# Performance work log

Measured on AMD Instinct MI355X. Metric: run time of the kernel, lower is better.

## Reference

```python
import jax, jax.numpy as jnp
import numpy as np

B, N, IN_DIM, OUT_DIM, H = 8, 1024, 256, 256, 8
D = OUT_DIM // H  # support_dim = 32


def setup_inputs() -> dict:
    key = jax.random.key(0)
    k_a, k_x, k_w, k_f1, k_f2 = jax.random.split(key, 5)
    A = (jax.random.uniform(k_a, (B, N, N)) < 0.05).astype(jnp.float32)
    eye = jnp.eye(N, dtype=jnp.float32)
    A = jnp.maximum(A, eye[None, :, :])
    X = jax.random.normal(k_x, (B, N, IN_DIM), dtype=jnp.float32)
    std_w = 1.0 / np.sqrt(OUT_DIM)
    std_f = 1.0 / np.sqrt(D)
    weight = jax.random.uniform(k_w, (IN_DIM, OUT_DIM), minval=-std_w, maxval=std_w)
    fc1 = jax.random.uniform(k_f1, (H, D), minval=-std_f, maxval=std_f)
    fc2 = jax.random.uniform(k_f2, (H, D), minval=-std_f, maxval=std_f)
    return {"A": A, "X": X, "weight": weight, "fc1": fc1, "fc2": fc2}


def reference(A, X, weight, fc1, fc2):
    # inputs: [B, N, H, D]
    inputs = jnp.einsum('bni,io->bno', X, weight).reshape(B, N, H, D)
    # additive attention scores (rank-1 broadcast)
    self_s = jnp.einsum('bnhd,hd->bhn', inputs, fc1)   # [B,H,N] (query/self term)
    neigh_s = jnp.einsum('bnhd,hd->bhn', inputs, fc2)  # [B,H,N] (key/neighbor term)
    scores = jax.nn.leaky_relu(self_s[:, :, :, None] + neigh_s[:, :, None, :])  # [B,H,N,N]
    mask = (-1e9 * (1.0 - A))[:, None, :, :]  # [B,1,N,N]
    alphas = jax.nn.softmax(scores + mask, axis=-1)  # [B,H,N,N]
    out = jnp.einsum('bhnm,bmhd->bnhd', alphas, inputs).reshape(B, N, OUT_DIM)
    return jax.nn.relu(out)
```

## Files before the change

kernel.cpp:

```cpp
#include <hip/hip_runtime.h>

typedef unsigned short u16;
typedef __attribute__((ext_vector_type(8))) short short8;
typedef __attribute__((ext_vector_type(4))) float floatx4;

#define NB 8
#define NN 1024
#define KDIM 256
#define ODIM 256
#define NH 8
#define BR 32
#define LDA 264
#define GWPB 4
#define GCAP 192

__device__ __forceinline__ u16 bf_rne(float x) {
    union { float f; unsigned u; } c{x};
    unsigned r = c.u + 0x7fff + ((c.u >> 16) & 1);
    return (u16)(r >> 16);
}
__device__ __forceinline__ float bf_f(u16 b) {
    union { unsigned u; float f; } c{(unsigned)b << 16};
    return c.f;
}
#define SPLIT1(val, A_, B_) { u16 hh_ = bf_rne(val); u16 ll_ = bf_rne((val) - bf_f(hh_)); A_ = hh_; B_ = ll_; }

__global__ __launch_bounds__(256) void wprep(const float* __restrict__ W,
                                             u16* __restrict__ WhiT,
                                             u16* __restrict__ WloT) {
    __shared__ float tile[64][65];
    int bt = blockIdx.x;
    int kt = bt >> 2, ot = bt & 3;
    int tid = threadIdx.x;
    int r = tid >> 6, c = tid & 63;
#pragma unroll
    for (int rr = r; rr < 64; rr += 4)
        tile[rr][c] = W[(kt * 64 + rr) * ODIM + ot * 64 + c];
    __syncthreads();
#pragma unroll
    for (int oo = r; oo < 64; oo += 4) {
        float w = tile[c][oo];
        u16 h, l;
        SPLIT1(w, h, l)
        WhiT[(ot * 64 + oo) * KDIM + kt * 64 + c] = h;
        WloT[(ot * 64 + oo) * KDIM + kt * 64 + c] = l;
    }
}

__global__ __launch_bounds__(256) void gemm_scores(
        const float* __restrict__ X, const u16* __restrict__ WhiT,
        const u16* __restrict__ WloT, const float* __restrict__ fc1,
        const float* __restrict__ fc2, u16* __restrict__ inp,
        float* __restrict__ self_t, float* __restrict__ neigh_t) {
    __shared__ u16 ah_lds[BR * LDA];
    __shared__ u16 al_lds[BR * LDA];

    int tid = threadIdx.x;
    int w = tid >> 6, lane = tid & 63;
    int m = lane & 15, q = lane >> 4;
    int bid = blockIdx.x;
    int row0 = (bid >> 1) * BR;
    int cbase = (bid & 1) * 128;

    const float4* Xr = (const float4*)(X + (size_t)row0 * KDIM);
#pragma unroll
    for (int p = 0; p < 8; ++p) {
        int f = p * 256 + tid;
        int r = f >> 6, c4 = (f & 63) * 4;
        float4 v = Xr[f];
        ushort4 hi, lo;
        SPLIT1(v.x, hi.x, lo.x)
        SPLIT1(v.y, hi.y, lo.y)
        SPLIT1(v.z, hi.z, lo.z)
        SPLIT1(v.w, hi.w, lo.w)
        *(ushort4*)&ah_lds[r * LDA + c4] = hi;
        *(ushort4*)&al_lds[r * LDA + c4] = lo;
    }
    __syncthreads();

    floatx4 acc[2][2] = {{{0,0,0,0},{0,0,0,0}},{{0,0,0,0},{0,0,0,0}}};
#pragma unroll
    for (int k0 = 0; k0 < KDIM; k0 += 32) {
        short8 Ah0 = *(const short8*)&ah_lds[m * LDA + k0 + q * 8];
        short8 Al0 = *(const short8*)&al_lds[m * LDA + k0 + q * 8];
        short8 Ah1 = *(const short8*)&ah_lds[(16 + m) * LDA + k0 + q * 8];
        short8 Al1 = *(const short8*)&al_lds[(16 + m) * LDA + k0 + q * 8];
#pragma unroll
        for (int t = 0; t < 2; ++t) {
            int o = cbase + w * 32 + t * 16 + m;
            short8 Bh = *(const short8*)(WhiT + (size_t)o * KDIM + k0 + q * 8);
            short8 Bl = *(const short8*)(WloT + (size_t)o * KDIM + k0 + q * 8);
            acc[0][t] = __builtin_amdgcn_mfma_f32_16x16x32_bf16(Ah0, Bh, acc[0][t], 0, 0, 0);
            acc[0][t] = __builtin_amdgcn_mfma_f32_16x16x32_bf16(Ah0, Bl, acc[0][t], 0, 0, 0);
            acc[0][t] = __builtin_amdgcn_mfma_f32_16x16x32_bf16(Al0, Bh, acc[0][t], 0, 0, 0);
            acc[1][t] = __builtin_amdgcn_mfma_f32_16x16x32_bf16(Ah1, Bh, acc[1][t], 0, 0, 0);
            acc[1][t] = __builtin_amdgcn_mfma_f32_16x16x32_bf16(Ah1, Bl, acc[1][t], 0, 0, 0);
            acc[1][t] = __builtin_amdgcn_mfma_f32_16x16x32_bf16(Al1, Bh, acc[1][t], 0, 0, 0);
        }
    }

#pragma unroll
    for (int rt = 0; rt < 2; ++rt)
#pragma unroll
        for (int t = 0; t < 2; ++t) {
            int col = cbase + w * 32 + t * 16 + m;
#pragma unroll
            for (int r = 0; r < 4; ++r)
                inp[(size_t)(row0 + rt * 16 + q * 4 + r) * ODIM + col] =
                    bf_rne(acc[rt][t][r]);
        }

    int hd = (bid & 1) * 4 + w;
    float f1[2], f2[2];
#pragma unroll
    for (int t = 0; t < 2; ++t) {
        int cl = hd * 32 + t * 16 + m;
        f1[t] = fc1[cl];
        f2[t] = fc2[cl];
    }
#pragma unroll
    for (int rt = 0; rt < 2; ++rt)
#pragma unroll
        for (int r = 0; r < 4; ++r) {
            float a = acc[rt][0][r] * f1[0] + acc[rt][1][r] * f1[1];
            float bb = acc[rt][0][r] * f2[0] + acc[rt][1][r] * f2[1];
#pragma unroll
            for (int ofs = 8; ofs >= 1; ofs >>= 1) {
                a += __shfl_xor(a, ofs);
                bb += __shfl_xor(bb, ofs);
            }
            if (m == 0) {
                int n = row0 + rt * 16 + q * 4 + r;
                self_t [(size_t)n * NH + hd] = a;
                neigh_t[(size_t)n * NH + hd] = bb;
            }
        }
}

__global__ __launch_bounds__(256) void gat_agg(
        const float* __restrict__ A, const u16* __restrict__ inp,
        const float* __restrict__ self_t, const float* __restrict__ neigh_t,
        float* __restrict__ out) {
    __shared__ u16 lst[GWPB][GCAP];

    int tid = threadIdx.x;
    int wv = tid >> 6, lane = tid & 63;
    int bx = blockIdx.x;
    int b = bx & 7;
    int n = ((bx >> 3) << 2) | wv;
    int bn = (b << 10) | n;

    const float4* Ar = (const float4*)(A + (size_t)bn * NN);
    float4 ac0 = Ar[lane];
    float4 ac1 = Ar[64 + lane];
    float4 ac2 = Ar[128 + lane];
    float4 ac3 = Ar[192 + lane];

    unsigned long long lt = (1ull << lane) - 1;
    u16* L = lst[wv];
    int total = 0;

#define COMPACT(V, EIDX) {                                                   \
        unsigned long long mk_ = __ballot((V) != 0.f);                       \
        if ((V) != 0.f) {                                                    \
            int p_ = total + __popcll(mk_ & lt);                             \
            if (p_ < GCAP) L[p_] = (u16)(EIDX);                              \
        }                                                                    \
        total += __popcll(mk_); }

    {
        int e0 = lane * 4;
        COMPACT(ac0.x, e0)       COMPACT(ac0.y, e0 + 1)
        COMPACT(ac0.z, e0 + 2)   COMPACT(ac0.w, e0 + 3)
        COMPACT(ac1.x, 256 + e0) COMPACT(ac1.y, 256 + e0 + 1)
        COMPACT(ac1.z, 256 + e0 + 2) COMPACT(ac1.w, 256 + e0 + 3)
        COMPACT(ac2.x, 512 + e0) COMPACT(ac2.y, 512 + e0 + 1)
        COMPACT(ac2.z, 512 + e0 + 2) COMPACT(ac2.w, 512 + e0 + 3)
        COMPACT(ac3.x, 768 + e0) COMPACT(ac3.y, 768 + e0 + 1)
        COMPACT(ac3.z, 768 + e0 + 2) COMPACT(ac3.w, 768 + e0 + 3)
    }
#undef COMPACT
    if (total > GCAP) total = GCAP;

    int hh = lane >> 3;
    float selfv = self_t[(size_t)bn * NH + hh];
    const float* nst = neigh_t + (size_t)(b << 10) * NH + hh;
    const ushort4* ib = (const ushort4*)(inp + ((size_t)(b << 10)) * ODIM) + lane;
    float sum = 0.f;
    floatx4 acc = {0.f, 0.f, 0.f, 0.f};
#pragma unroll 4
    for (int i = 0; i < total; ++i) {
        int idx = L[i];
        float s = selfv + nst[(size_t)idx * NH];
        s = s > 0.f ? s : 0.01f * s;
        float e = __expf(s);
        sum += e;
        ushort4 v = ib[(size_t)idx * 64];
        acc[0] = fmaf(e, bf_f(v.x), acc[0]);
        acc[1] = fmaf(e, bf_f(v.y), acc[1]);
        acc[2] = fmaf(e, bf_f(v.z), acc[2]);
        acc[3] = fmaf(e, bf_f(v.w), acc[3]);
    }

    float inv = 1.f / sum;
    float4 o;
    o.x = acc[0] * inv; o.y = acc[1] * inv;
    o.z = acc[2] * inv; o.w = acc[3] * inv;
    o.x = o.x > 0.f ? o.x : 0.f;
    o.y = o.y > 0.f ? o.y : 0.f;
    o.z = o.z > 0.f ? o.z : 0.f;
    o.w = o.w > 0.f ? o.w : 0.f;
    *(float4*)(out + (size_t)bn * ODIM + lane * 4) = o;
}

extern "C" void kernel_launch(void* const* d_in, const int* in_sizes, int n_in,
                              void* d_out, int out_size, void* d_ws, size_t ws_size,
                              hipStream_t stream) {
    const float* A   = (const float*)d_in[0];
    const float* X   = (const float*)d_in[1];
    const float* W   = (const float*)d_in[2];
    const float* fc1 = (const float*)d_in[3];
    const float* fc2 = (const float*)d_in[4];
    float* out = (float*)d_out;

    char* ws = (char*)d_ws;
    const size_t MB = 1024u * 1024u;
    u16*   inp     = (u16*)ws;
    u16*   WhiT    = (u16*)(ws + 4 * MB);
    u16*   WloT    = (u16*)(ws + 4 * MB + 128 * 1024);
    float* self_t  = (float*)(ws + 4 * MB + 256 * 1024);
    float* neigh_t = (float*)(ws + 4 * MB + 512 * 1024);

    wprep<<<16, 256, 0, stream>>>(W, WhiT, WloT);
    gemm_scores<<<(NB * NN / BR) * 2, 256, 0, stream>>>(
        X, WhiT, WloT, fc1, fc2, inp, self_t, neigh_t);
    gat_agg<<<NB * NN / GWPB, 256, 0, stream>>>(A, inp, self_t, neigh_t, out);
}
```

Baseline: 123.2 us.

## Fuse weight prep, GEMM and aggregation into one cooperative persistent kernel

Merges the three kernels into a single cooperative launch of 512 blocks separated by grid-wide syncs, so there is only one kernel launch. The aggregation phase now has each wave handle four rows in sequence, prefetching the next adjacency row while the current one is compacted and aggregated. This removes inter-kernel launch gaps but adds grid barrier cost, leaves most blocks idle during the weight-prep phase, and reduces parallelism in the aggregation phase.

```diff
diff --git a/kernel.cpp b/kernel.cpp
--- a/kernel.cpp
+++ b/kernel.cpp
@@ -1,4 +1,7 @@
 #include <hip/hip_runtime.h>
+#include <hip/hip_cooperative_groups.h>
+
+namespace cg = cooperative_groups;
 
 typedef unsigned short u16;
 typedef __attribute__((ext_vector_type(8))) short short8;
@@ -11,7 +14,6 @@
 #define NH 8
 #define BR 32
 #define LDA 264
-#define GWPB 4
 #define GCAP 192
 
 __device__ __forceinline__ u16 bf_rne(float x) {
@@ -25,192 +27,200 @@
 }
 #define SPLIT1(val, A_, B_) { u16 hh_ = bf_rne(val); u16 ll_ = bf_rne((val) - bf_f(hh_)); A_ = hh_; B_ = ll_; }
 
-__global__ __launch_bounds__(256) void wprep(const float* __restrict__ W,
-                                             u16* __restrict__ WhiT,
-                                             u16* __restrict__ WloT) {
-    __shared__ float tile[64][65];
-    int bt = blockIdx.x;
-    int kt = bt >> 2, ot = bt & 3;
+__global__ __launch_bounds__(256, 2) void gat_fused(
+        const float* __restrict__ A, const float* __restrict__ X,
+        const float* __restrict__ W, const float* __restrict__ fc1,
+        const float* __restrict__ fc2, u16* __restrict__ inp,
+        u16* __restrict__ WhiT, u16* __restrict__ WloT,
+        float* __restrict__ self_t, float* __restrict__ neigh_t,
+        float* __restrict__ out) {
+    __shared__ __align__(16) char smem[2 * BR * LDA * 2];
+
     int tid = threadIdx.x;
-    int r = tid >> 6, c = tid & 63;
-#pragma unroll
-    for (int rr = r; rr < 64; rr += 4)
-        tile[rr][c] = W[(kt * 64 + rr) * ODIM + ot * 64 + c];
-    __syncthreads();
-#pragma unroll
-    for (int oo = r; oo < 64; oo += 4) {
-        float w = tile[c][oo];
-        u16 h, l;
-        SPLIT1(w, h, l)
-        WhiT[(ot * 64 + oo) * KDIM + kt * 64 + c] = h;
-        WloT[(ot * 64 + oo) * KDIM + kt * 64 + c] = l;
+    int bid = blockIdx.x;
+    int w = tid >> 6, lane = tid & 63;
+
+    if (bid < 16) {
+        float (*tile)[65] = (float(*)[65])smem;
+        int kt = bid >> 2, ot = bid & 3;
+        int r = tid >> 6, c = tid & 63;
+#pragma unroll
+        for (int rr = r; rr < 64; rr += 4)
+            tile[rr][c] = W[(kt * 64 + rr) * ODIM + ot * 64 + c];
+        __syncthreads();
+#pragma unroll
+        for (int oo = r; oo < 64; oo += 4) {
+            float wv_ = tile[c][oo];
+            u16 h, l;
+            SPLIT1(wv_, h, l)
+            WhiT[(ot * 64 + oo) * KDIM + kt * 64 + c] = h;
+            WloT[(ot * 64 + oo) * KDIM + kt * 64 + c] = l;
+        }
+        __threadfence();
     }
-}
-
-__global__ __launch_bounds__(256) void gemm_scores(
-        const float* __restrict__ X, const u16* __restrict__ WhiT,
-        const u16* __restrict__ WloT, const float* __restrict__ fc1,
-        const float* __restrict__ fc2, u16* __restrict__ inp,
-        float* __restrict__ self_t, float* __restrict__ neigh_t) {
-    __shared__ u16 ah_lds[BR * LDA];
-    __shared__ u16 al_lds[BR * LDA];
-
-    int tid = threadIdx.x;
-    int w = tid >> 6, lane = tid & 63;
-    int m = lane & 15, q = lane >> 4;
-    int bid = blockIdx.x;
-    int row0 = (bid >> 1) * BR;
-    int cbase = (bid & 1) * 128;
-
-    const float4* Xr = (const float4*)(X + (size_t)row0 * KDIM);
-#pragma unroll
-    for (int p = 0; p < 8; ++p) {
-        int f = p * 256 + tid;
-        int r = f >> 6, c4 = (f & 63) * 4;
-        float4 v = Xr[f];
-        ushort4 hi, lo;
-        SPLIT1(v.x, hi.x, lo.x)
-        SPLIT1(v.y, hi.y, lo.y)
-        SPLIT1(v.z, hi.z, lo.z)
-        SPLIT1(v.w, hi.w, lo.w)
-        *(ushort4*)&ah_lds[r * LDA + c4] = hi;
-        *(ushort4*)&al_lds[r * LDA + c4] = lo;
+    cg::this_grid().sync();
+
+    {
+        u16* ah_lds = (u16*)smem;
+        u16* al_lds = (u16*)smem + BR * LDA;
+
+        int m = lane & 15, q = lane >> 4;
+        int row0 = (bid >> 1) * BR;
+        int cbase = (bid & 1) * 128;
+
+        const float4* Xr = (const float4*)(X + (size_t)row0 * KDIM);
+#pragma unroll
+        for (int p = 0; p < 8; ++p) {
+            int f = p * 256 + tid;
+            int r = f >> 6, c4 = (f & 63) * 4;
+            float4 v = Xr[f];
+            ushort4 hi, lo;
+            SPLIT1(v.x, hi.x, lo.x)
+            SPLIT1(v.y, hi.y, lo.y)
+            SPLIT1(v.z, hi.z, lo.z)
+            SPLIT1(v.w, hi.w, lo.w)
+            *(ushort4*)&ah_lds[r * LDA + c4] = hi;
+            *(ushort4*)&al_lds[r * LDA + c4] = lo;
+        }
+        __syncthreads();
+
+        floatx4 acc[2][2] = {{{0,0,0,0},{0,0,0,0}},{{0,0,0,0},{0,0,0,0}}};
+#pragma unroll
+        for (int k0 = 0; k0 < KDIM; k0 += 32) {
+            short8 Ah0 = *(const short8*)&ah_lds[m * LDA + k0 + q * 8];
+            short8 Al0 = *(const short8*)&al_lds[m * LDA + k0 + q * 8];
+            short8 Ah1 = *(const short8*)&ah_lds[(16 + m) * LDA + k0 + q * 8];
+            short8 Al1 = *(const short8*)&al_lds[(16 + m) * LDA + k0 + q * 8];
+#pragma unroll
+            for (int t = 0; t < 2; ++t) {
+                int o = cbase + w * 32 + t * 16 + m;
+                short8 Bh = *(const short8*)(WhiT + (size_t)o * KDIM + k0 + q * 8);
+                short8 Bl = *(const short8*)(WloT + (size_t)o * KDIM + k0 + q * 8);
+                acc[0][t] = __builtin_amdgcn_mfma_f32_16x16x32_bf16(Ah0, Bh, acc[0][t], 0, 0, 0);
+                acc[0][t] = __builtin_amdgcn_mfma_f32_16x16x32_bf16(Ah0, Bl, acc[0][t], 0, 0, 0);
+                acc[0][t] = __builtin_amdgcn_mfma_f32_16x16x32_bf16(Al0, Bh, acc[0][t], 0, 0, 0);
+                acc[1][t] = __builtin_amdgcn_mfma_f32_16x16x32_bf16(Ah1, Bh, acc[1][t], 0, 0, 0);
+                acc[1][t] = __builtin_amdgcn_mfma_f32_16x16x32_bf16(Ah1, Bl, acc[1][t], 0, 0, 0);
+                acc[1][t] = __builtin_amdgcn_mfma_f32_16x16x32_bf16(Al1, Bh, acc[1][t], 0, 0, 0);
+            }
+        }
+
+#pragma unroll
+        for (int rt = 0; rt < 2; ++rt)
+#pragma unroll
+            for (int t = 0; t < 2; ++t) {
+                int col = cbase + w * 32 + t * 16 + m;
+#pragma unroll
+                for (int r = 0; r < 4; ++r)
+                    inp[(size_t)(row0 + rt * 16 + q * 4 + r) * ODIM + col] =
+                        bf_rne(acc[rt][t][r]);
+            }
+
+        int hd = (bid & 1) * 4 + w;
+        float f1[2], f2[2];
+#pragma unroll
+        for (int t = 0; t < 2; ++t) {
+            int cl = hd * 32 + t * 16 + m;
+            f1[t] = fc1[cl];
+            f2[t] = fc2[cl];
+        }
+#pragma unroll
+        for (int rt = 0; rt < 2; ++rt)
+#pragma unroll
+            for (int r = 0; r < 4; ++r) {
+                float a = acc[rt][0][r] * f1[0] + acc[rt][1][r] * f1[1];
+                float bb = acc[rt][0][r] * f2[0] + acc[rt][1][r] * f2[1];
+#pragma unroll
+                for (int ofs = 8; ofs >= 1; ofs >>= 1) {
+                    a += __shfl_xor(a, ofs);
+                    bb += __shfl_xor(bb, ofs);
+                }
+                if (m == 0) {
+                    int n = row0 + rt * 16 + q * 4 + r;
+                    self_t [(size_t)n * NH + hd] = a;
+                    neigh_t[(size_t)n * NH + hd] = bb;
+                }
+            }
+        __threadfence();
     }
-    __syncthreads();
-
-    floatx4 acc[2][2] = {{{0,0,0,0},{0,0,0,0}},{{0,0,0,0},{0,0,0,0}}};
-#pragma unroll
-    for (int k0 = 0; k0 < KDIM; k0 += 32) {
-        short8 Ah0 = *(const short8*)&ah_lds[m * LDA + k0 + q * 8];
-        short8 Al0 = *(const short8*)&al_lds[m * LDA + k0 + q * 8];
-        short8 Ah1 = *(const short8*)&ah_lds[(16 + m) * LDA + k0 + q * 8];
-        short8 Al1 = *(const short8*)&al_lds[(16 + m) * LDA + k0 + q * 8];
-#pragma unroll
-        for (int t = 0; t < 2; ++t) {
-            int o = cbase + w * 32 + t * 16 + m;
-            short8 Bh = *(const short8*)(WhiT + (size_t)o * KDIM + k0 + q * 8);
-            short8 Bl = *(const short8*)(WloT + (size_t)o * KDIM + k0 + q * 8);
-            acc[0][t] = __builtin_amdgcn_mfma_f32_16x16x32_bf16(Ah0, Bh, acc[0][t], 0, 0, 0);
-            acc[0][t] = __builtin_amdgcn_mfma_f32_16x16x32_bf16(Ah0, Bl, acc[0][t], 0, 0, 0);
-            acc[0][t] = __builtin_amdgcn_mfma_f32_16x16x32_bf16(Al0, Bh, acc[0][t], 0, 0, 0);
-            acc[1][t] = __builtin_amdgcn_mfma_f32_16x16x32_bf16(Ah1, Bh, acc[1][t], 0, 0, 0);
-            acc[1][t] = __builtin_amdgcn_mfma_f32_16x16x32_bf16(Ah1, Bl, acc[1][t], 0, 0, 0);
-            acc[1][t] = __builtin_amdgcn_mfma_f32_16x16x32_bf16(Al1, Bh, acc[1][t], 0, 0, 0);
+    cg::this_grid().sync();
+
+    {
+        u16* L = (u16*)smem + w * GCAP;
+        unsigned long long lt = (1ull << lane) - 1;
+        int hh = lane >> 3;
+        int b = (bid * 16) >> 10;
+        const float* nstb = neigh_t + (size_t)(b << 10) * NH + hh;
+        const ushort4* ib = (const ushort4*)(inp + ((size_t)(b << 10)) * ODIM) + lane;
+
+        int bn = bid * 16 + w;
+        float4 c0, c1, c2, c3;
+        {
+            const float4* Ar = (const float4*)(A + (size_t)bn * NN);
+            c0 = Ar[lane]; c1 = Ar[64 + lane]; c2 = Ar[128 + lane]; c3 = Ar[192 + lane];
+        }
+
+#pragma unroll
+        for (int j = 0; j < 4; ++j) {
+            float4 n0 = c0, n1 = c1, n2 = c2, n3 = c3;
+            if (j < 3) {
+                const float4* Ar = (const float4*)(A + (size_t)(bn + 4) * NN);
+                n0 = Ar[lane]; n1 = Ar[64 + lane]; n2 = Ar[128 + lane]; n3 = Ar[192 + lane];
+            }
+
+            int total = 0;
+#define COMPACT(V, EIDX) {                                                   \
+            unsigned long long mk_ = __ballot((V) != 0.f);                   \
+            if ((V) != 0.f) {                                                \
+                int p_ = total + __popcll(mk_ & lt);                         \
+                if (p_ < GCAP) L[p_] = (u16)(EIDX);                          \
+            }                                                                \
+            total += __popcll(mk_); }
+            {
+                int e0 = lane * 4;
+                COMPACT(c0.x, e0)           COMPACT(c0.y, e0 + 1)
+                COMPACT(c0.z, e0 + 2)       COMPACT(c0.w, e0 + 3)
+                COMPACT(c1.x, 256 + e0)     COMPACT(c1.y, 256 + e0 + 1)
+                COMPACT(c1.z, 256 + e0 + 2) COMPACT(c1.w, 256 + e0 + 3)
+                COMPACT(c2.x, 512 + e0)     COMPACT(c2.y, 512 + e0 + 1)
+                COMPACT(c2.z, 512 + e0 + 2) COMPACT(c2.w, 512 + e0 + 3)
+                COMPACT(c3.x, 768 + e0)     COMPACT(c3.y, 768 + e0 + 1)
+                COMPACT(c3.z, 768 + e0 + 2) COMPACT(c3.w, 768 + e0 + 3)
+            }
+#undef COMPACT
+            if (total > GCAP) total = GCAP;
+
+            float selfv = self_t[(size_t)bn * NH + hh];
+            float sum = 0.f;
+            floatx4 acc = {0.f, 0.f, 0.f, 0.f};
+#pragma unroll 4
+            for (int i = 0; i < total; ++i) {
+                int idx = L[i];
+                float s = selfv + nstb[(size_t)idx * NH];
+                s = s > 0.f ? s : 0.01f * s;
+                float e = __expf(s);
+                sum += e;
+                ushort4 v = ib[(size_t)idx * 64];
+                acc[0] = fmaf(e, bf_f(v.x), acc[0]);
+                acc[1] = fmaf(e, bf_f(v.y), acc[1]);
+                acc[2] = fmaf(e, bf_f(v.z), acc[2]);
+                acc[3] = fmaf(e, bf_f(v.w), acc[3]);
+            }
+
+            float inv = 1.f / sum;
+            float4 o;
+            o.x = acc[0] * inv; o.y = acc[1] * inv;
+            o.z = acc[2] * inv; o.w = acc[3] * inv;
+            o.x = o.x > 0.f ? o.x : 0.f;
+            o.y = o.y > 0.f ? o.y : 0.f;
+            o.z = o.z > 0.f ? o.z : 0.f;
+            o.w = o.w > 0.f ? o.w : 0.f;
+            *(float4*)(out + (size_t)bn * ODIM + lane * 4) = o;
+
+            c0 = n0; c1 = n1; c2 = n2; c3 = n3;
+            bn += 4;
         }
     }
-
-#pragma unroll
-    for (int rt = 0; rt < 2; ++rt)
-#pragma unroll
-        for (int t = 0; t < 2; ++t) {
-            int col = cbase + w * 32 + t * 16 + m;
-#pragma unroll
-            for (int r = 0; r < 4; ++r)
-                inp[(size_t)(row0 + rt * 16 + q * 4 + r) * ODIM + col] =
-                    bf_rne(acc[rt][t][r]);
-        }
-
-    int hd = (bid & 1) * 4 + w;
-    float f1[2], f2[2];
-#pragma unroll
-    for (int t = 0; t < 2; ++t) {
-        int cl = hd * 32 + t * 16 + m;
-        f1[t] = fc1[cl];
-        f2[t] = fc2[cl];
-    }
-#pragma unroll
-    for (int rt = 0; rt < 2; ++rt)
-#pragma unroll
-        for (int r = 0; r < 4; ++r) {
-            float a = acc[rt][0][r] * f1[0] + acc[rt][1][r] * f1[1];
-            float bb = acc[rt][0][r] * f2[0] + acc[rt][1][r] * f2[1];
-#pragma unroll
-            for (int ofs = 8; ofs >= 1; ofs >>= 1) {
-                a += __shfl_xor(a, ofs);
-                bb += __shfl_xor(bb, ofs);
-            }
-            if (m == 0) {
-                int n = row0 + rt * 16 + q * 4 + r;
-                self_t [(size_t)n * NH + hd] = a;
-                neigh_t[(size_t)n * NH + hd] = bb;
-            }
-        }
-}
-
-__global__ __launch_bounds__(256) void gat_agg(
-        const float* __restrict__ A, const u16* __restrict__ inp,
-        const float* __restrict__ self_t, const float* __restrict__ neigh_t,
-        float* __restrict__ out) {
-    __shared__ u16 lst[GWPB][GCAP];
-
-    int tid = threadIdx.x;
-    int wv = tid >> 6, lane = tid & 63;
-    int bx = blockIdx.x;
-    int b = bx & 7;
-    int n = ((bx >> 3) << 2) | wv;
-    int bn = (b << 10) | n;
-
-    const float4* Ar = (const float4*)(A + (size_t)bn * NN);
-    float4 ac0 = Ar[lane];
-    float4 ac1 = Ar[64 + lane];
-    float4 ac2 = Ar[128 + lane];
-    float4 ac3 = Ar[192 + lane];
-
-    unsigned long long lt = (1ull << lane) - 1;
-    u16* L = lst[wv];
-    int total = 0;
-
-#define COMPACT(V, EIDX) {                                                   \
-        unsigned long long mk_ = __ballot((V) != 0.f);                       \
-        if ((V) != 0.f) {                                                    \
-            int p_ = total + __popcll(mk_ & lt);                             \
-            if (p_ < GCAP) L[p_] = (u16)(EIDX);                              \
-        }                                                                    \
-        total += __popcll(mk_); }
-
-    {
-        int e0 = lane * 4;
-        COMPACT(ac0.x, e0)       COMPACT(ac0.y, e0 + 1)
-        COMPACT(ac0.z, e0 + 2)   COMPACT(ac0.w, e0 + 3)
-        COMPACT(ac1.x, 256 + e0) COMPACT(ac1.y, 256 + e0 + 1)
-        COMPACT(ac1.z, 256 + e0 + 2) COMPACT(ac1.w, 256 + e0 + 3)
-        COMPACT(ac2.x, 512 + e0) COMPACT(ac2.y, 512 + e0 + 1)
-        COMPACT(ac2.z, 512 + e0 + 2) COMPACT(ac2.w, 512 + e0 + 3)
-        COMPACT(ac3.x, 768 + e0) COMPACT(ac3.y, 768 + e0 + 1)
-        COMPACT(ac3.z, 768 + e0 + 2) COMPACT(ac3.w, 768 + e0 + 3)
-    }
-#undef COMPACT
-    if (total > GCAP) total = GCAP;
-
-    int hh = lane >> 3;
-    float selfv = self_t[(size_t)bn * NH + hh];
-    const float* nst = neigh_t + (size_t)(b << 10) * NH + hh;
-    const ushort4* ib = (const ushort4*)(inp + ((size_t)(b << 10)) * ODIM) + lane;
-    float sum = 0.f;
-    floatx4 acc = {0.f, 0.f, 0.f, 0.f};
-#pragma unroll 4
-    for (int i = 0; i < total; ++i) {
-        int idx = L[i];
-        float s = selfv + nst[(size_t)idx * NH];
-        s = s > 0.f ? s : 0.01f * s;
-        float e = __expf(s);
-        sum += e;
-        ushort4 v = ib[(size_t)idx * 64];
-        acc[0] = fmaf(e, bf_f(v.x), acc[0]);
-        acc[1] = fmaf(e, bf_f(v.y), acc[1]);
-        acc[2] = fmaf(e, bf_f(v.z), acc[2]);
-        acc[3] = fmaf(e, bf_f(v.w), acc[3]);
-    }
-
-    float inv = 1.f / sum;
-    float4 o;
-    o.x = acc[0] * inv; o.y = acc[1] * inv;
-    o.z = acc[2] * inv; o.w = acc[3] * inv;
-    o.x = o.x > 0.f ? o.x : 0.f;
-    o.y = o.y > 0.f ? o.y : 0.f;
-    o.z = o.z > 0.f ? o.z : 0.f;
-    o.w = o.w > 0.f ? o.w : 0.f;
-    *(float4*)(out + (size_t)bn * ODIM + lane * 4) = o;
 }
 
 extern "C" void kernel_launch(void* const* d_in, const int* in_sizes, int n_in,
@@ -231,8 +241,9 @@
     float* self_t  = (float*)(ws + 4 * MB + 256 * 1024);
     float* neigh_t = (float*)(ws + 4 * MB + 512 * 1024);
 
-    wprep<<<16, 256, 0, stream>>>(W, WhiT, WloT);
-    gemm_scores<<<(NB * NN / BR) * 2, 256, 0, stream>>>(
-        X, WhiT, WloT, fc1, fc2, inp, self_t, neigh_t);
-    gat_agg<<<NB * NN / GWPB, 256, 0, stream>>>(A, inp, self_t, neigh_t, out);
-}
+    void* args[] = {(void*)&A, (void*)&X, (void*)&W, (void*)&fc1, (void*)&fc2,
+                    (void*)&inp, (void*)&WhiT, (void*)&WloT,
+                    (void*)&self_t, (void*)&neigh_t, (void*)&out};
+    hipLaunchCooperativeKernel(reinterpret_cast<void*>(gat_fused),
+                               dim3(512), dim3(256), args, 0, stream);
+}
```

Measured after the change: 297.6 us. 142% more time.
